# Optimization experiments

Measured on AMD Instinct MI355X. Metric: run time of the kernel, lower is better.

## Reference

```python
import jax, jax.numpy as jnp
import numpy as np

EPS = 1e-5
K = 3  # fixed kernel_size in the module


def _conv(x, w, pad):
    return jax.lax.conv_general_dilated(
        x, w, (1, 1), [(pad, pad), (pad, pad)],
        dimension_numbers=('NCHW', 'OIHW', 'NCHW'))


def _bn(x, g, b, m, v):
    # inference-mode BatchNorm2d with running stats
    scale = g / jnp.sqrt(v + EPS)
    return x * scale[None, :, None, None] + (b - m * scale)[None, :, None, None]


def _unfold3(x):
    # x: [B,C,H,W] -> [B,C,9,H,W]; kernel positions row-major, matching nn.Unfold
    H, W = x.shape[2], x.shape[3]
    xp = jnp.pad(x, ((0, 0), (0, 0), (1, 1), (1, 1)))
    return jnp.stack([xp[:, :, i:i + H, j:j + W]
                      for i in range(K) for j in range(K)], axis=2)


def setup_inputs() -> dict:
    key = jax.random.key(0)
    ks = jax.random.split(key, 9)
    B, C, H, W = 8, 64, 128, 128
    Cr = C // 4           # reduce channels = 16
    KN = K * K * 2        # kernel_num = 18 (groups = 2)
    guide_feat = jax.random.normal(ks[0], (B, C, H, W), jnp.float32)
    target_feat = jax.random.normal(ks[1], (B, C, H, W), jnp.float32)
    w_reduce = jax.random.normal(ks[2], (Cr, C, 1, 1), jnp.float32) * 0.1
    bn1_g = jnp.ones((Cr,), jnp.float32)
    bn1_b = jnp.zeros((Cr,), jnp.float32)
    bn1_m = jax.random.normal(ks[3], (Cr,), jnp.float32) * 0.1
    bn1_v = jax.random.uniform(ks[4], (Cr,), jnp.float32, 0.5, 1.5)
    w_span = jax.random.normal(ks[5], (KN, Cr, 1, 1), jnp.float32) * 0.1
    b_span = jnp.zeros((KN,), jnp.float32)
    w_bconv = jax.random.normal(ks[6], (C, C, 3, 3), jnp.float32) * 0.05
    bn3_g = jnp.ones((C,), jnp.float32)
    bn3_b = jnp.zeros((C,), jnp.float32)
    bn3_m = jax.random.normal(ks[7], (C,), jnp.float32) * 0.1
    bn3_v = jax.random.uniform(ks[8], (C,), jnp.float32, 0.5, 1.5)
    return dict(guide_feat=guide_feat, target_feat=target_feat,
                w_reduce=w_reduce, bn1_g=bn1_g, bn1_b=bn1_b, bn1_m=bn1_m, bn1_v=bn1_v,
                w_span=w_span, b_span=b_span,
                w_bconv=w_bconv, bn3_g=bn3_g, bn3_b=bn3_b, bn3_m=bn3_m, bn3_v=bn3_v)


def reference(guide_feat, target_feat, w_reduce, bn1_g, bn1_b, bn1_m, bn1_v,
              w_span, b_span, w_bconv, bn3_g, bn3_b, bn3_m, bn3_v):
    B, C, H, W = target_feat.shape
    groups = 2
    gc = C // 2  # group_channels
    # kernel generation branch
    x = guide_feat + target_feat
    x = jax.nn.relu(_bn(_conv(x, w_reduce, 0), bn1_g, bn1_b, bn1_m, bn1_v))
    kern = _conv(x, w_span, 0) + b_span[None, :, None, None]  # [B,18,H,W]
    kern = kern.reshape(B, groups, K * K, H, W)
    # involution: unfold target, multiply by per-pixel kernels, sum over window
    patches = _unfold3(target_feat).reshape(B, groups, gc, K * K, H, W)
    out = jnp.einsum('bgkhw,bgckhw->bgchw', kern, patches).reshape(B, C, H, W)
    # final 3x3 ConvBNReLU
    return jax.nn.relu(_bn(_conv(out, w_bconv, 1), bn3_g, bn3_b, bn3_m, bn3_v))
```

## Files before the change

kernel.cpp:

```cpp
#include <hip/hip_runtime.h>

#define B_  8
#define C_  64
#define H_  128
#define W_  128
#define HW_ (H_*W_)
#define NP_ ((size_t)B_*HW_)

typedef __attribute__((ext_vector_type(4)))  float f32x4;
typedef __attribute__((ext_vector_type(16))) float f32x16;
typedef __attribute__((ext_vector_type(8)))  short short8;

static __device__ __forceinline__ unsigned short f2bf(float f) {
  unsigned int u = __float_as_uint(f);
  u += 0x7fff + ((u >> 16) & 1);
  return (unsigned short)(u >> 16);
}
static __device__ __forceinline__ float bf2f(unsigned short u) {
  return __uint_as_float((unsigned int)u << 16);
}

__global__ void k0_prep(const float* __restrict__ w,
                        const float* __restrict__ g3, const float* __restrict__ b3,
                        const float* __restrict__ m3, const float* __restrict__ v3,
                        unsigned short* __restrict__ afrag,
                        float* __restrict__ s3, float* __restrict__ sh3) {
  int idx = blockIdx.x * 256 + threadIdx.x;
  if (idx < 36864) {
    int j    = idx & 7;
    int lane = (idx >> 3) & 63;
    int fs   = idx >> 9;
    int ks16 = fs & 3;
    int kk   = (fs >> 2) % 9;
    int mh   = fs / 36;
    int oc = mh * 32 + (lane & 31);
    int ic = ks16 * 16 + (lane >> 5) * 8 + j;
    afrag[idx] = f2bf(w[(oc * 64 + ic) * 9 + kk]);
  } else if (idx < 36864 + 64) {
    int c = idx - 36864;
    float s = g3[c] * rsqrtf(v3[c] + 1e-5f);
    s3[c]  = s;
    sh3[c] = b3[c] - m3[c] * s;
  }
}

__global__ __launch_bounds__(256) void k1_fused(
    const float* __restrict__ guide, const float* __restrict__ target,
    const float* __restrict__ w_reduce, const float* __restrict__ bn1g,
    const float* __restrict__ bn1b, const float* __restrict__ bn1m,
    const float* __restrict__ bn1v, const float* __restrict__ w_span,
    const float* __restrict__ b_span, unsigned short* __restrict__ inv) {
  __shared__ __align__(16) unsigned short t16[324 * 64];
  __shared__ f32x4 s_wred[64][4];
  __shared__ f32x4 s_wspan[18][4];
  __shared__ float s_s1[16], s_sh1[16], s_bsp[18];
  int t = threadIdx.x;
  for (int i = t; i < 1024; i += 256) {
    int c = i >> 4, r = i & 15;
    ((float*)&s_wred[c][0])[r] = w_reduce[r * 64 + c];
  }
  for (int i = t; i < 288; i += 256) {
    int j = i / 16, r = i % 16;
    ((float*)&s_wspan[j][0])[r] = w_span[j * 16 + r];
  }
  if (t < 16) {
    float s = bn1g[t] * rsqrtf(bn1v[t] + 1e-5f);
    s_s1[t]  = s;
    s_sh1[t] = bn1b[t] - bn1m[t] * s;
  }
  if (t < 18) s_bsp[t] = b_span[t];

  int b  = blockIdx.z;
  int h0 = blockIdx.y * 16, w0 = blockIdx.x * 16;
  const float* tb = target + (size_t)b * C_ * HW_;

  for (int i = t; i < 2592; i += 256) {
    int c8 = i / 324, cell = i - c8 * 324;
    int r = cell / 18, col = cell - r * 18;
    int hh = h0 + r - 1, ww = w0 + col - 1;
    short8 val = {0, 0, 0, 0, 0, 0, 0, 0};
    if ((unsigned)hh < (unsigned)H_ && (unsigned)ww < (unsigned)W_) {
      const float* src = tb + (size_t)(c8 * 8) * HW_ + hh * W_ + ww;
      #pragma unroll
      for (int ci = 0; ci < 8; ++ci) val[ci] = (short)f2bf(src[(size_t)ci * HW_]);
    }
    *(short8*)&t16[cell * 64 + ((c8 ^ (cell & 7)) * 8)] = val;
  }
  __syncthreads();

  int ty = t >> 4, tx = t & 15;
  const float* gp = guide + (size_t)b * C_ * HW_ + (h0 + ty) * W_ + (w0 + tx);
  int cell1 = (ty + 1) * 18 + (tx + 1);

  f32x4 xr[4];
  xr[0] = 0.f; xr[1] = 0.f; xr[2] = 0.f; xr[3] = 0.f;
  #pragma unroll
  for (int c8 = 0; c8 < 8; ++c8) {
    short8 tv = *(const short8*)&t16[cell1 * 64 + ((c8 ^ (cell1 & 7)) * 8)];
    #pragma unroll
    for (int ci = 0; ci < 8; ++ci) {
      int c = c8 * 8 + ci;
      float v = gp[(size_t)c * HW_] + bf2f((unsigned short)tv[ci]);
      #pragma unroll
      for (int q = 0; q < 4; ++q) xr[q] += s_wred[c][q] * v;
    }
  }
  #pragma unroll
  for (int q = 0; q < 4; ++q) {
    #pragma unroll
    for (int r = 0; r < 4; ++r) {
      float x = xr[q][r] * s_s1[q * 4 + r] + s_sh1[q * 4 + r];
      xr[q][r] = fmaxf(x, 0.f);
    }
  }
  float kern[18];
  #pragma unroll
  for (int j = 0; j < 18; ++j) {
    f32x4 a = s_wspan[j][0] * xr[0] + s_wspan[j][1] * xr[1]
            + s_wspan[j][2] * xr[2] + s_wspan[j][3] * xr[3];
    kern[j] = s_bsp[j] + a[0] + a[1] + a[2] + a[3];
  }

  size_t pix = ((size_t)b * H_ + (h0 + ty)) * W_ + (w0 + tx);
  #pragma unroll
  for (int c8 = 0; c8 < 8; ++c8) {
    const float* kb = &kern[(c8 >> 2) * 9];
    float acc[8];
    #pragma unroll
    for (int ci = 0; ci < 8; ++ci) acc[ci] = 0.f;
    #pragma unroll
    for (int di = 0; di < 3; ++di) {
      #pragma unroll
      for (int dj = 0; dj < 3; ++dj) {
        int cell = (ty + di) * 18 + (tx + dj);
        short8 tv = *(const short8*)&t16[cell * 64 + ((c8 ^ (cell & 7)) * 8)];
        float k = kb[di * 3 + dj];
        #pragma unroll
        for (int ci = 0; ci < 8; ++ci) acc[ci] += k * bf2f((unsigned short)tv[ci]);
      }
    }
    short8 pv;
    #pragma unroll
    for (int ci = 0; ci < 8; ++ci) pv[ci] = (short)f2bf(acc[ci]);
    *(short8*)(inv + ((size_t)c8 * NP_ + pix) * 8) = pv;
  }
}

__global__ __launch_bounds__(256, 4) void k2_conv(
    const unsigned short* __restrict__ inv, const unsigned short* __restrict__ afrag,
    const float* __restrict__ s3g, const float* __restrict__ sh3g,
    float* __restrict__ out) {
  __shared__ __align__(16) unsigned short tile[204 * 64];
  int t = threadIdx.x;
  int b  = blockIdx.z;
  int h0 = blockIdx.y * 4;
  int w0 = blockIdx.x * 32;

  #pragma unroll
  for (int chunk = 0; chunk < 8; ++chunk) {
    if (t < 204) {
      int r = t / 34, col = t - r * 34;
      int hh = h0 + r - 1, ww = w0 + col - 1;
      short8 val = {0, 0, 0, 0, 0, 0, 0, 0};
      if ((unsigned)hh < (unsigned)H_ && (unsigned)ww < (unsigned)W_)
        val = *(const short8*)(inv + ((size_t)chunk * NP_ + ((size_t)b * H_ + hh) * W_ + ww) * 8);
      *(short8*)&tile[t * 64 + ((chunk ^ (col & 7)) * 8)] = val;
    }
  }

  int wave = t >> 6, lane = t & 63;
  int mh = wave & 1;
  int rp = (wave >> 1) * 2;
  __syncthreads();

  f32x16 acc0, acc1;
  #pragma unroll
  for (int i = 0; i < 16; ++i) { acc0[i] = 0.f; acc1[i] = 0.f; }

  for (int kk = 0; kk < 9; ++kk) {
    int di = kk / 3, dj = kk - di * 3;
    const unsigned short* ap = afrag + (((size_t)(mh * 9 + kk) * 4) * 64 + lane) * 8;
    short8 A0 = *(const short8*)(ap);
    short8 A1 = *(const short8*)(ap + 512);
    short8 A2 = *(const short8*)(ap + 1024);
    short8 A3 = *(const short8*)(ap + 1536);
    int col = (lane & 31) + dj;
    int swb = (lane >> 5);
    int cb0 = (rp + di) * 34 + col;
    #pragma unroll
    for (int ks = 0; ks < 4; ++ks) {
      int sw = ((ks * 2 + swb) ^ (col & 7)) * 8;
      short8 b0 = *(const short8*)&tile[cb0 * 64 + sw];
      short8 b1 = *(const short8*)&tile[(cb0 + 34) * 64 + sw];
      short8 Ak = (ks == 0) ? A0 : (ks == 1) ? A1 : (ks == 2) ? A2 : A3;
      acc0 = __builtin_amdgcn_mfma_f32_32x32x16_bf16(Ak, b0, acc0, 0, 0, 0);
      acc1 = __builtin_amdgcn_mfma_f32_32x32x16_bf16(Ak, b1, acc1, 0, 0, 0);
    }
  }

  int wcol = lane & 31;
  #pragma unroll
  for (int reg = 0; reg < 16; ++reg) {
    int oc = mh * 32 + (reg & 3) + 8 * (reg >> 2) + 4 * (lane >> 5);
    float s  = s3g[oc];
    float sh = sh3g[oc];
    float* op = out + ((size_t)b * C_ + oc) * HW_ + (h0 + rp) * W_ + w0 + wcol;
    op[0]  = fmaxf(acc0[reg] * s + sh, 0.f);
    op[W_] = fmaxf(acc1[reg] * s + sh, 0.f);
  }
}

extern "C" void kernel_launch(void* const* d_in, const int* in_sizes, int n_in,
                              void* d_out, int out_size, void* d_ws, size_t ws_size,
                              hipStream_t stream) {
  const float* guide    = (const float*)d_in[0];
  const float* target   = (const float*)d_in[1];
  const float* w_reduce = (const float*)d_in[2];
  const float* bn1g     = (const float*)d_in[3];
  const float* bn1b     = (const float*)d_in[4];
  const float* bn1m     = (const float*)d_in[5];
  const float* bn1v     = (const float*)d_in[6];
  const float* w_span   = (const float*)d_in[7];
  const float* b_span   = (const float*)d_in[8];
  const float* w_bconv  = (const float*)d_in[9];
  const float* bn3g     = (const float*)d_in[10];
  const float* bn3b     = (const float*)d_in[11];
  const float* bn3m     = (const float*)d_in[12];
  const float* bn3v     = (const float*)d_in[13];
  float* out = (float*)d_out;

  unsigned short* afrag = (unsigned short*)d_ws;
  float* s3  = (float*)((char*)d_ws + 73728);
  float* sh3 = (float*)((char*)d_ws + 73728 + 256);
  unsigned short* inv   = (unsigned short*)((char*)d_ws + (1 << 17));

  hipLaunchKernelGGL(k0_prep, dim3(145), dim3(256), 0, stream,
                     w_bconv, bn3g, bn3b, bn3m, bn3v, afrag, s3, sh3);
  hipLaunchKernelGGL(k1_fused, dim3(W_ / 16, H_ / 16, B_), dim3(256), 0, stream,
                     guide, target, w_reduce, bn1g, bn1b, bn1m, bn1v,
                     w_span, b_span, inv);
  hipLaunchKernelGGL(k2_conv, dim3(W_ / 32, H_ / 4, B_), dim3(256), 0, stream,
                     inv, afrag, s3, sh3, out);
}
```

Baseline: 166.2 us.

## Compute reduce conv with MFMA and split pixels across wave halves

The 1x1 reduce convolution in the fused kernel now runs as a bf16 MFMA against a prepacked weight fragment built in the prep kernel, replacing the scalar FMA loop. The block grows to 512 threads, and each pixel is handled by two half-waves that split the channel groups and exchange partial span-kernel sums through a cross-lane shuffle. This is meant to cut VALU work and per-thread register load in the kernel-generation stage. In exchange, the reduce input and the padded 16 output rows of the MFMA are rounded to bf16, which adds rounding error.

```diff
diff --git a/kernel.cpp b/kernel.cpp
--- a/kernel.cpp
+++ b/kernel.cpp
@@ -20,10 +20,11 @@
   return __uint_as_float((unsigned int)u << 16);
 }
 
-__global__ void k0_prep(const float* __restrict__ w,
+__global__ void k0_prep(const float* __restrict__ w, const float* __restrict__ wred,
                         const float* __restrict__ g3, const float* __restrict__ b3,
                         const float* __restrict__ m3, const float* __restrict__ v3,
                         unsigned short* __restrict__ afrag,
+                        unsigned short* __restrict__ afrag_red,
                         float* __restrict__ s3, float* __restrict__ sh3) {
   int idx = blockIdx.x * 256 + threadIdx.x;
   if (idx < 36864) {
@@ -36,37 +37,42 @@
     int oc = mh * 32 + (lane & 31);
     int ic = ks16 * 16 + (lane >> 5) * 8 + j;
     afrag[idx] = f2bf(w[(oc * 64 + ic) * 9 + kk]);
-  } else if (idx < 36864 + 64) {
-    int c = idx - 36864;
+  } else if (idx < 38912) {
+    int i2 = idx - 36864;
+    int j    = i2 & 7;
+    int lane = (i2 >> 3) & 63;
+    int ks   = i2 >> 9;
+    int m  = lane & 31;
+    int ic = ks * 16 + (lane >> 5) * 8 + j;
+    afrag_red[i2] = (m < 16) ? f2bf(wred[m * 64 + ic]) : (unsigned short)0;
+  } else if (idx < 38976) {
+    int c = idx - 38912;
     float s = g3[c] * rsqrtf(v3[c] + 1e-5f);
     s3[c]  = s;
     sh3[c] = b3[c] - m3[c] * s;
   }
 }
 
-__global__ __launch_bounds__(256) void k1_fused(
+__global__ __launch_bounds__(512, 4) void k1_fused(
     const float* __restrict__ guide, const float* __restrict__ target,
-    const float* __restrict__ w_reduce, const float* __restrict__ bn1g,
-    const float* __restrict__ bn1b, const float* __restrict__ bn1m,
-    const float* __restrict__ bn1v, const float* __restrict__ w_span,
-    const float* __restrict__ b_span, unsigned short* __restrict__ inv) {
+    const unsigned short* __restrict__ afrag_red,
+    const float* __restrict__ bn1g, const float* __restrict__ bn1b,
+    const float* __restrict__ bn1m, const float* __restrict__ bn1v,
+    const float* __restrict__ w_span, const float* __restrict__ b_span,
+    unsigned short* __restrict__ inv) {
   __shared__ __align__(16) unsigned short t16[324 * 64];
-  __shared__ f32x4 s_wred[64][4];
   __shared__ f32x4 s_wspan[18][4];
-  __shared__ float s_s1[16], s_sh1[16], s_bsp[18];
+  __shared__ f32x4 s_s1v[4], s_sh1v[4];
+  __shared__ float s_bsp[18];
   int t = threadIdx.x;
-  for (int i = t; i < 1024; i += 256) {
-    int c = i >> 4, r = i & 15;
-    ((float*)&s_wred[c][0])[r] = w_reduce[r * 64 + c];
-  }
-  for (int i = t; i < 288; i += 256) {
-    int j = i / 16, r = i % 16;
-    ((float*)&s_wspan[j][0])[r] = w_span[j * 16 + r];
+  if (t < 288) {
+    int j = t >> 4, r = t & 15;
+    ((float*)&s_wspan[j][0])[r] = w_span[t];
   }
   if (t < 16) {
     float s = bn1g[t] * rsqrtf(bn1v[t] + 1e-5f);
-    s_s1[t]  = s;
-    s_sh1[t] = bn1b[t] - bn1m[t] * s;
+    ((float*)s_s1v)[t]  = s;
+    ((float*)s_sh1v)[t] = bn1b[t] - bn1m[t] * s;
   }
   if (t < 18) s_bsp[t] = b_span[t];
 
@@ -74,7 +80,7 @@
   int h0 = blockIdx.y * 16, w0 = blockIdx.x * 16;
   const float* tb = target + (size_t)b * C_ * HW_;
 
-  for (int i = t; i < 2592; i += 256) {
+  for (int i = t; i < 2592; i += 512) {
     int c8 = i / 324, cell = i - c8 * 324;
     int r = cell / 18, col = cell - r * 18;
     int hh = h0 + r - 1, ww = w0 + col - 1;
@@ -86,62 +92,82 @@
     }
     *(short8*)&t16[cell * 64 + ((c8 ^ (cell & 7)) * 8)] = val;
   }
+
+  int wave = t >> 6, l = t & 63, h = l >> 5;
+  short8 a_red[4];
+  #pragma unroll
+  for (int ks = 0; ks < 4; ++ks)
+    a_red[ks] = *(const short8*)(afrag_red + ((size_t)(ks * 64 + l)) * 8);
   __syncthreads();
 
-  int ty = t >> 4, tx = t & 15;
-  const float* gp = guide + (size_t)b * C_ * HW_ + (h0 + ty) * W_ + (w0 + tx);
-  int cell1 = (ty + 1) * 18 + (tx + 1);
-
-  f32x4 xr[4];
-  xr[0] = 0.f; xr[1] = 0.f; xr[2] = 0.f; xr[3] = 0.f;
-  #pragma unroll
-  for (int c8 = 0; c8 < 8; ++c8) {
-    short8 tv = *(const short8*)&t16[cell1 * 64 + ((c8 ^ (cell1 & 7)) * 8)];
-    #pragma unroll
-    for (int ci = 0; ci < 8; ++ci) {
-      int c = c8 * 8 + ci;
-      float v = gp[(size_t)c * HW_] + bf2f((unsigned short)tv[ci]);
-      #pragma unroll
-      for (int q = 0; q < 4; ++q) xr[q] += s_wred[c][q] * v;
-    }
-  }
-  #pragma unroll
-  for (int q = 0; q < 4; ++q) {
+  int p   = wave * 32 + (l & 31);
+  int tyP = p >> 4, txP = p & 15;
+  const float* gpx = guide + (size_t)b * C_ * HW_ + (h0 + tyP) * W_ + (w0 + txP);
+  int cellC = (tyP + 1) * 18 + (txP + 1);
+
+  f32x16 xa;
+  #pragma unroll
+  for (int i = 0; i < 16; ++i) xa[i] = 0.f;
+  #pragma unroll
+  for (int ks = 0; ks < 4; ++ks) {
+    short8 tvv = *(const short8*)&t16[cellC * 64 + (((2 * ks + h) ^ (cellC & 7)) * 8)];
+    int ch0 = ks * 16 + h * 8;
+    short8 bf;
+    #pragma unroll
+    for (int j = 0; j < 8; ++j)
+      bf[j] = (short)f2bf(gpx[(size_t)(ch0 + j) * HW_] + bf2f((unsigned short)tvv[j]));
+    xa = __builtin_amdgcn_mfma_f32_32x32x16_bf16(a_red[ks], bf, xa, 0, 0, 0);
+  }
+  f32x4 x0, x1;
+  #pragma unroll
+  for (int r = 0; r < 4; ++r) { x0[r] = xa[r]; x1[r] = xa[4 + r]; }
+  {
+    f32x4 sA = s_s1v[h], shA = s_sh1v[h], sB = s_s1v[2 + h], shB = s_sh1v[2 + h];
     #pragma unroll
     for (int r = 0; r < 4; ++r) {
-      float x = xr[q][r] * s_s1[q * 4 + r] + s_sh1[q * 4 + r];
-      xr[q][r] = fmaxf(x, 0.f);
-    }
-  }
-  float kern[18];
-  #pragma unroll
-  for (int j = 0; j < 18; ++j) {
-    f32x4 a = s_wspan[j][0] * xr[0] + s_wspan[j][1] * xr[1]
-            + s_wspan[j][2] * xr[2] + s_wspan[j][3] * xr[3];
-    kern[j] = s_bsp[j] + a[0] + a[1] + a[2] + a[3];
-  }
-
-  size_t pix = ((size_t)b * H_ + (h0 + ty)) * W_ + (w0 + tx);
-  #pragma unroll
-  for (int c8 = 0; c8 < 8; ++c8) {
-    const float* kb = &kern[(c8 >> 2) * 9];
-    float acc[8];
-    #pragma unroll
-    for (int ci = 0; ci < 8; ++ci) acc[ci] = 0.f;
+      x0[r] = fmaxf(x0[r] * sA[r] + shA[r], 0.f);
+      x1[r] = fmaxf(x1[r] * sB[r] + shB[r], 0.f);
+    }
+  }
+
+  float kg[9];
+  #pragma unroll
+  for (int j9 = 0; j9 < 9; ++j9) {
+    int jA = h * 9 + j9;
+    int jB = (9 - 9 * h) + j9;
+    f32x4 wA0 = s_wspan[jA][h],     wA1 = s_wspan[jA][2 + h];
+    f32x4 wB0 = s_wspan[jB][h],     wB1 = s_wspan[jB][2 + h];
+    float pa = 0.f, pb = 0.f;
+    #pragma unroll
+    for (int r = 0; r < 4; ++r) {
+      pa += wA0[r] * x0[r] + wA1[r] * x1[r];
+      pb += wB0[r] * x0[r] + wB1[r] * x1[r];
+    }
+    float recv = __shfl_xor(pb, 32, 64);
+    kg[j9] = pa + recv + s_bsp[jA];
+  }
+
+  size_t pix = ((size_t)b * H_ + (h0 + tyP)) * W_ + (w0 + txP);
+  #pragma unroll
+  for (int i = 0; i < 4; ++i) {
+    int c8 = h * 4 + i;
+    float a8[8];
+    #pragma unroll
+    for (int ci = 0; ci < 8; ++ci) a8[ci] = 0.f;
     #pragma unroll
     for (int di = 0; di < 3; ++di) {
       #pragma unroll
       for (int dj = 0; dj < 3; ++dj) {
-        int cell = (ty + di) * 18 + (tx + dj);
+        int cell = (tyP + di) * 18 + (txP + dj);
         short8 tv = *(const short8*)&t16[cell * 64 + ((c8 ^ (cell & 7)) * 8)];
-        float k = kb[di * 3 + dj];
+        float k = kg[di * 3 + dj];
         #pragma unroll
-        for (int ci = 0; ci < 8; ++ci) acc[ci] += k * bf2f((unsigned short)tv[ci]);
+        for (int ci = 0; ci < 8; ++ci) a8[ci] += k * bf2f((unsigned short)tv[ci]);
       }
     }
     short8 pv;
     #pragma unroll
-    for (int ci = 0; ci < 8; ++ci) pv[ci] = (short)f2bf(acc[ci]);
+    for (int ci = 0; ci < 8; ++ci) pv[ci] = (short)f2bf(a8[ci]);
     *(short8*)(inv + ((size_t)c8 * NP_ + pix) * 8) = pv;
   }
 }
@@ -229,15 +255,17 @@
   const float* bn3v     = (const float*)d_in[13];
   float* out = (float*)d_out;
 
-  unsigned short* afrag = (unsigned short*)d_ws;
-  float* s3  = (float*)((char*)d_ws + 73728);
-  float* sh3 = (float*)((char*)d_ws + 73728 + 256);
-  unsigned short* inv   = (unsigned short*)((char*)d_ws + (1 << 17));
-
-  hipLaunchKernelGGL(k0_prep, dim3(145), dim3(256), 0, stream,
-                     w_bconv, bn3g, bn3b, bn3m, bn3v, afrag, s3, sh3);
-  hipLaunchKernelGGL(k1_fused, dim3(W_ / 16, H_ / 16, B_), dim3(256), 0, stream,
-                     guide, target, w_reduce, bn1g, bn1b, bn1m, bn1v,
+  unsigned short* afrag     = (unsigned short*)d_ws;
+  unsigned short* afrag_red = (unsigned short*)((char*)d_ws + 81920);
+  float* s3  = (float*)((char*)d_ws + 90112);
+  float* sh3 = (float*)((char*)d_ws + 90368);
+  unsigned short* inv = (unsigned short*)((char*)d_ws + (1 << 17));
+
+  hipLaunchKernelGGL(k0_prep, dim3(153), dim3(256), 0, stream,
+                     w_bconv, w_reduce, bn3g, bn3b, bn3m, bn3v,
+                     afrag, afrag_red, s3, sh3);
+  hipLaunchKernelGGL(k1_fused, dim3(W_ / 16, H_ / 16, B_), dim3(512), 0, stream,
+                     guide, target, afrag_red, bn1g, bn1b, bn1m, bn1v,
                      w_span, b_span, inv);
   hipLaunchKernelGGL(k2_conv, dim3(W_ / 32, H_ / 4, B_), dim3(256), 0, stream,
                      inv, afrag, s3, sh3, out);
```

Measured after the change: 164.5 us. About the same (-1.0%).
